# Performance work log

Measured on AMD Instinct MI355X. Metric: run time of the kernel, lower is better.

The kernel has to match this reference:

```python
import jax, jax.numpy as jnp
import numpy as np
import math

MAX_L = 3
E, R, C = 100000, 8, 16  # num_edges, n_radial, n_chanel


def _l_list(max_l):
    # all monomial exponent triples (lx,ly,lz) with lx+ly+lz <= max_l,
    # in the nested-loop order used for init_kwargs l_list
    return [(lx, ly, lz)
            for lx in range(max_l + 1)
            for ly in range(max_l + 1 - lx)
            for lz in range(max_l + 1 - lx - ly)]


def _combo_indices(max_l):
    # find_combo_vectors_l1l2: for every l3 in l_list, every componentwise
    # decomposition l3 = l1 + l2, with integer binomial prefactor
    ll = _l_list(max_l)
    idx = {t: i for i, t in enumerate(ll)}
    l3s, l1s, l2s, pf = [], [], [], []
    for l3 in ll:
        for a in range(l3[0] + 1):
            for b in range(l3[1] + 1):
                for c in range(l3[2] + 1):
                    l1 = (a, b, c)
                    l2 = (l3[0] - a, l3[1] - b, l3[2] - c)
                    l3s.append(idx[l3])
                    l1s.append(idx[l1])
                    l2s.append(idx[l2])
                    pf.append(math.comb(l3[0], a) * math.comb(l3[1], b) * math.comb(l3[2], c))
    return (np.asarray(l3s, np.int32), np.asarray(l1s, np.int32),
            np.asarray(l2s, np.int32), np.asarray(pf, np.float32))


def setup_inputs() -> dict:
    key = jax.random.key(0)
    k1, k2 = jax.random.split(key)
    A = len(_l_list(MAX_L))  # n_angular = 20
    edge_attr1 = jax.random.normal(k1, (E, R, A, C), dtype=jnp.float32)
    edge_attr2 = jax.random.normal(k2, (E, R, A, C), dtype=jnp.float32)
    l3_idx, l1_idx, l2_idx, prefactor = _combo_indices(MAX_L)
    return {
        "edge_attr1": edge_attr1,
        "edge_attr2": edge_attr2,
        "l3_idx": jnp.asarray(l3_idx),
        "l1_idx": jnp.asarray(l1_idx),
        "l2_idx": jnp.asarray(l2_idx),
        "prefactor": jnp.asarray(prefactor),
    }


def reference(edge_attr1, edge_attr2, l3_idx, l1_idx, l2_idx, prefactor):
    # vectorized gather-multiply-scale over all K=84 (l1,l2,l3) combos,
    # then one scatter-add into the l3 angular slot
    terms = (prefactor[None, None, :, None]
             * edge_attr1[:, :, l1_idx, :]
             * edge_attr2[:, :, l2_idx, :])  # [E, R, K, C]
    out = jnp.zeros_like(edge_attr1).at[:, :, l3_idx, :].add(terms)
    return out
```

## Files before the change

### kernel.cpp

```cpp
#include <hip/hip_runtime.h>


#define NA 20
#define NK 84
#define TR 8
#define ROWQ 80
#define PADQ 82
#define NTH 128

typedef float f32x4 __attribute__((ext_vector_type(4)));

namespace atp {

constexpr int lidx(int x, int y, int z) {
  int i = 0;
  for (int a = 0; a < x; ++a) i += (4 - a) * (5 - a) / 2;
  for (int b = 0; b < y; ++b) i += 4 - x - b;
  return i + z;
}

constexpr int combi(int n, int k) {
  int r = 1;
  for (int i = 1; i <= k; ++i) r = r * (n - k + i) / i;
  return r;
}

struct Tab {
  int l1[NK];
  int l2[NK];
  float pf[NK];
  int cnt[NA];
  int off[NA];
};

constexpr Tab make_tab() {
  Tab t{};
  int n = 0, m = 0;
  for (int x = 0; x <= 3; ++x)
    for (int y = 0; y <= 3 - x; ++y)
      for (int z = 0; z <= 3 - x - y; ++z) {
        t.off[m] = n;
        t.cnt[m] = (x + 1) * (y + 1) * (z + 1);
        for (int a = 0; a <= x; ++a)
          for (int b = 0; b <= y; ++b)
            for (int c = 0; c <= z; ++c) {
              t.l1[n] = lidx(a, b, c);
              t.l2[n] = lidx(x - a, y - b, z - c);
              t.pf[n] = (float)(combi(x, a) * combi(y, b) * combi(z, c));
              ++n;
            }
        ++m;
      }
  return t;
}

constexpr Tab T = make_tab();

}

__global__ __launch_bounds__(NTH) void atp_kernel(
    const float* __restrict__ in1, const float* __restrict__ in2,
    float* __restrict__ out) {
  __shared__ f32x4 lds1[TR * PADQ];
  __shared__ f32x4 lds2[TR * PADQ];

  const int t = threadIdx.x;
  const long base_q = (long)blockIdx.x * (TR * ROWQ);
  const f32x4* g1 = reinterpret_cast<const f32x4*>(in1) + base_q;
  const f32x4* g2 = reinterpret_cast<const f32x4*>(in2) + base_q;

#pragma unroll
  for (int k = 0; k < 5; ++k) {
    const int q = k * NTH + t;
    const int row = q / ROWQ;
    const int qq = q - row * ROWQ;
    lds1[row * PADQ + qq] = g1[q];
    lds2[row * PADQ + qq] = g2[q];
  }
  __syncthreads();

  const int row = t >> 4;
  const int c = t & 15;
  const float* l1p = reinterpret_cast<const float*>(lds1) + row * (PADQ * 4) + c;
  const float* l2p = reinterpret_cast<const float*>(lds2) + row * (PADQ * 4) + c;
  float* op = out + base_q * 4 + row * (ROWQ * 4) + c;

  float v1[NA], v2[NA];
#pragma unroll
  for (int a = 0; a < NA; ++a) v1[a] = l1p[a * 16];
#pragma unroll
  for (int a = 0; a < NA; ++a) v2[a] = l2p[a * 16];

#pragma unroll
  for (int i3 = 0; i3 < NA; ++i3) {
    float acc = 0.f;
#pragma unroll
    for (int j = 0; j < atp::T.cnt[i3]; ++j) {
      const int k = atp::T.off[i3] + j;
      acc = fmaf(atp::T.pf[k] * v1[atp::T.l1[k]], v2[atp::T.l2[k]], acc);
    }
    op[i3 * 16] = acc;
  }
}

extern "C" void kernel_launch(void* const* d_in, const int* in_sizes, int n_in,
                              void* d_out, int out_size, void* d_ws, size_t ws_size,
                              hipStream_t stream) {
  const float* in1 = (const float*)d_in[0];
  const float* in2 = (const float*)d_in[1];
  float* out = (float*)d_out;
  const int n_tiles = out_size / (TR * NA * 16);
  atp_kernel<<<n_tiles, NTH, 0, stream>>>(in1, in2, out);
}
```

Measured before the change: 545.1 us.

## Use persistent grid-stride blocks with register prefetch of next tile

The kernel moves from one block per tile to a fixed grid of persistent blocks that stride over tiles. Each block loads the next tile's inputs into registers while it computes the current tile from LDS, so global loads overlap with compute. This cuts block launch overhead and hides load latency, but it adds register pressure, an extra barrier per tile, and fewer concurrent blocks to hide memory latency.

```diff
diff --git a/kernel.cpp b/kernel.cpp
--- a/kernel.cpp
+++ b/kernel.cpp
@@ -7,6 +7,7 @@
 #define ROWQ 80
 #define PADQ 82
 #define NTH 128
+#define NBLK 1792
 
 typedef float f32x4 __attribute__((ext_vector_type(4)));
 
@@ -60,46 +61,78 @@
 
 __global__ __launch_bounds__(NTH) void atp_kernel(
     const float* __restrict__ in1, const float* __restrict__ in2,
-    float* __restrict__ out) {
+    float* __restrict__ out, int n_tiles) {
   __shared__ f32x4 lds1[TR * PADQ];
   __shared__ f32x4 lds2[TR * PADQ];
 
   const int t = threadIdx.x;
-  const long base_q = (long)blockIdx.x * (TR * ROWQ);
-  const f32x4* g1 = reinterpret_cast<const f32x4*>(in1) + base_q;
-  const f32x4* g2 = reinterpret_cast<const f32x4*>(in2) + base_q;
+  const int stride = gridDim.x;
 
+  int srow[5], sqq[5];
 #pragma unroll
   for (int k = 0; k < 5; ++k) {
     const int q = k * NTH + t;
-    const int row = q / ROWQ;
-    const int qq = q - row * ROWQ;
-    lds1[row * PADQ + qq] = g1[q];
-    lds2[row * PADQ + qq] = g2[q];
+    srow[k] = q / ROWQ;
+    sqq[k] = q - srow[k] * ROWQ;
   }
-  __syncthreads();
-
   const int row = t >> 4;
   const int c = t & 15;
   const float* l1p = reinterpret_cast<const float*>(lds1) + row * (PADQ * 4) + c;
   const float* l2p = reinterpret_cast<const float*>(lds2) + row * (PADQ * 4) + c;
-  float* op = out + base_q * 4 + row * (ROWQ * 4) + c;
 
-  float v1[NA], v2[NA];
+  long tile = blockIdx.x;
+  const f32x4* g1 = reinterpret_cast<const f32x4*>(in1) + tile * (TR * ROWQ);
+  const f32x4* g2 = reinterpret_cast<const f32x4*>(in2) + tile * (TR * ROWQ);
+
+  f32x4 r1[5], r2[5];
 #pragma unroll
-  for (int a = 0; a < NA; ++a) v1[a] = l1p[a * 16];
+  for (int k = 0; k < 5; ++k) {
+    const int q = k * NTH + t;
+    r1[k] = g1[q];
+    r2[k] = g2[q];
+  }
+
+  while (tile < n_tiles) {
 #pragma unroll
-  for (int a = 0; a < NA; ++a) v2[a] = l2p[a * 16];
+    for (int k = 0; k < 5; ++k) {
+      lds1[srow[k] * PADQ + sqq[k]] = r1[k];
+      lds2[srow[k] * PADQ + sqq[k]] = r2[k];
+    }
+    __syncthreads();
 
+    const long next = tile + stride;
+    if (next < n_tiles) {
+      const f32x4* n1 = g1 + (long)stride * (TR * ROWQ);
+      const f32x4* n2 = g2 + (long)stride * (TR * ROWQ);
 #pragma unroll
-  for (int i3 = 0; i3 < NA; ++i3) {
-    float acc = 0.f;
+      for (int k = 0; k < 5; ++k) {
+        const int q = k * NTH + t;
+        r1[k] = n1[q];
+        r2[k] = n2[q];
+      }
+      g1 = n1;
+      g2 = n2;
+    }
+
+    float v1[NA], v2[NA];
 #pragma unroll
-    for (int j = 0; j < atp::T.cnt[i3]; ++j) {
-      const int k = atp::T.off[i3] + j;
-      acc = fmaf(atp::T.pf[k] * v1[atp::T.l1[k]], v2[atp::T.l2[k]], acc);
+    for (int a = 0; a < NA; ++a) v1[a] = l1p[a * 16];
+#pragma unroll
+    for (int a = 0; a < NA; ++a) v2[a] = l2p[a * 16];
+
+    float* op = out + tile * (TR * ROWQ * 4) + row * (ROWQ * 4) + c;
+#pragma unroll
+    for (int i3 = 0; i3 < NA; ++i3) {
+      float acc = 0.f;
+#pragma unroll
+      for (int j = 0; j < atp::T.cnt[i3]; ++j) {
+        const int k = atp::T.off[i3] + j;
+        acc = fmaf(atp::T.pf[k] * v1[atp::T.l1[k]], v2[atp::T.l2[k]], acc);
+      }
+      op[i3 * 16] = acc;
     }
-    op[i3 * 16] = acc;
+    __syncthreads();
+    tile = next;
   }
 }
 
@@ -110,5 +143,6 @@
   const float* in2 = (const float*)d_in[1];
   float* out = (float*)d_out;
   const int n_tiles = out_size / (TR * NA * 16);
-  atp_kernel<<<n_tiles, NTH, 0, stream>>>(in1, in2, out);
+  const int blocks = n_tiles < NBLK ? n_tiles : NBLK;
+  atp_kernel<<<blocks, NTH, 0, stream>>>(in1, in2, out, n_tiles);
 }
```

Result: slower. 619.9 us (+13.7%).
